# Kernel tuning notes

Hardware: AMD Instinct MI355X
Metric: run time of the kernel (lower is better)

Reference implementation:

```python
import jax, jax.numpy as jnp
import numpy as np

NEG_INF = -1e9  # matches torch masked_fill(-1000000000.0)


def setup_inputs() -> dict:
    key = jax.random.key(0)
    kv, kk, kq, km, kw, kb = jax.random.split(key, 6)
    B, Lq, Lk, D = 8, 1024, 4096, 1024  # Lq must equal D (transpose-then-merge quirk)
    v = jax.random.normal(kv, (B, Lk, D), dtype=jnp.float32)
    k = jax.random.normal(kk, (B, Lk, D), dtype=jnp.float32)
    q = jax.random.normal(kq, (B, Lq, D), dtype=jnp.float32)
    mask = jax.random.randint(km, (B, Lq, Lk), 0, 2) > 0  # bool, True = masked out
    W_merge = jax.random.normal(kw, (D, D), dtype=jnp.float32) / np.sqrt(D)
    b_merge = jax.random.normal(kb, (D,), dtype=jnp.float32) * 0.02
    return {"v": v, "k": k, "q": q, "mask": mask, "W_merge": W_merge, "b_merge": b_merge}


def reference(v, k, q, mask, W_merge, b_merge):
    d_k = q.shape[-1]
    scale = 1.0 / jnp.sqrt(jnp.asarray(d_k, dtype=q.dtype))
    # scores: [B, Lq, Lk]
    scores = jnp.einsum('bqd,bkd->bqk', q, k) * scale
    scores = jnp.where(mask, jnp.asarray(NEG_INF, dtype=scores.dtype), scores)
    att_map = jax.nn.softmax(scores, axis=-1)  # dropout = identity in eval
    atted = jnp.einsum('bqk,bkd->bqd', att_map, v)  # [B, Lq, D]
    atted = jnp.swapaxes(atted, -1, -2)  # [B, D, Lq]; Lq == hid_dim
    # nn.Linear: y = x @ W^T + b
    return jnp.einsum('bdl,ol->bdo', atted, W_merge) + b_merge
```

## Files before the change

kernel.cpp:

```cpp
#include <hip/hip_runtime.h>
#include <stdint.h>

typedef __attribute__((ext_vector_type(4))) float f32x4;
typedef __attribute__((ext_vector_type(8))) short bf16x8;
typedef __attribute__((ext_vector_type(4))) short bf16x4v;
typedef __attribute__((ext_vector_type(4))) unsigned int u32x4;

#define NBATCH 8
#define LQS    1024
#define LKS    4096
#define DDIM   1024
#define QKSCALE 0.03125f
#define NEGINF -1000000000.0f
#define BK 64

__device__ __forceinline__ short f2bf(float x) {
    unsigned u = __builtin_bit_cast(unsigned, x);
    unsigned r = (u + 0x7fffu + ((u >> 16) & 1u)) >> 16;
    return (short)r;
}
__device__ __forceinline__ float bf2f(short s) {
    unsigned u = ((unsigned)(unsigned short)s) << 16;
    return __builtin_bit_cast(float, u);
}

__device__ __forceinline__ bf16x8 cvt8(const float* f) {
    const u32x4* u = (const u32x4*)f;
    const u32x4 a = u[0], b = u[1];
    union { unsigned w[4]; bf16x8 v; } c;
    c.w[0] = __builtin_amdgcn_perm(a[1], a[0], 0x07060302u);
    c.w[1] = __builtin_amdgcn_perm(a[3], a[2], 0x07060302u);
    c.w[2] = __builtin_amdgcn_perm(b[1], b[0], 0x07060302u);
    c.w[3] = __builtin_amdgcn_perm(b[3], b[2], 0x07060302u);
    return c.v;
}

__device__ __forceinline__ void g2l16(const void* g, void* lds) {
    __builtin_amdgcn_global_load_lds(
        (const __attribute__((address_space(1))) unsigned int*)g,
        (__attribute__((address_space(3))) unsigned int*)lds,
        16, 0, 0);
}

__device__ __forceinline__ int xcd_swz(int bid, int nwg) {
    return (bid & 7) * (nwg >> 3) + (bid >> 3);
}

__global__ void detect_kernel(const unsigned char* __restrict__ mb,
                              int* __restrict__ flags) {
    if (threadIdx.x != 0 || blockIdx.x != 0) return;
    int is_i32 = 1;
    for (int i = 0; i < 256; ++i) {
        if ((i & 3) != 0 && mb[i] != 0) { is_i32 = 0; break; }
    }
    flags[0] = is_i32;
}

__global__ __launch_bounds__(256) void cvt_kernel(
    const float* __restrict__ src, short* __restrict__ dst, int n8) {
    const int stride = gridDim.x * 256;
    for (int i = blockIdx.x * 256 + threadIdx.x; i < n8; i += stride)
        ((bf16x8*)dst)[i] = cvt8(src + (size_t)i * 8);
}

__global__ __launch_bounds__(256) void transv_kernel(
    const float* __restrict__ V, short* __restrict__ VT) {
    __shared__ short LDSt[64 * 72];
    const int tid = threadIdx.x;
    const int cb  = blockIdx.x >> 10;
    const int t   = blockIdx.x & 1023;
    const int kt  = t >> 4, dt = t & 15;
    const int k0  = kt * 64, d0 = dt * 64;
    const float* Vb  = V  + (size_t)cb * LKS * DDIM;
    short*       VTb = VT + (size_t)cb * ((size_t)DDIM * LKS);

    const int r  = tid >> 4;
    const int cp = (tid & 15) * 4;
#pragma unroll
    for (int rr = 0; rr < 4; ++rr) {
        const int row = rr * 16 + r;
        const f32x4 v = *(const f32x4*)(Vb + (size_t)(k0 + row) * DDIM + d0 + cp);
#pragma unroll
        for (int i = 0; i < 4; ++i) LDSt[(cp + i) * 72 + row] = f2bf(v[i]);
    }
    __syncthreads();
    const int dr = tid >> 2;
    const int kq = (tid & 3) * 16;
    const bf16x8 o0 = *(const bf16x8*)&LDSt[dr * 72 + kq];
    const bf16x8 o1 = *(const bf16x8*)&LDSt[dr * 72 + kq + 8];
    short* dst = VTb + (size_t)(d0 + dr) * LKS + k0 + kq;
    *(bf16x8*)dst       = o0;
    *(bf16x8*)(dst + 8) = o1;
}

__device__ __forceinline__ void stage_half(const short* gbase, int ld,
                                           short* ldshalf, int tid) {
    const int r0 = tid >> 3;
    const int gc = (tid & 7) ^ (r0 & 7);
    const short* s0 = gbase + (size_t)r0 * ld + gc * 8;
    const short* s1 = gbase + (size_t)(r0 + 64) * ld + gc * 8;
    g2l16(s0, ldshalf + (tid & 0x1C0) * 8);
    g2l16(s1, ldshalf + 4096 + (tid & 0x1C0) * 8);
}

__device__ __forceinline__ bf16x8 rdfrag(const short* lds, int base, int r, int c) {
    return *(const bf16x8*)&lds[base + r * 64 + ((c ^ (r & 7)) << 3)];
}

#define MFMA16(d, a, b) d = __builtin_amdgcn_mfma_f32_16x16x32_bf16(a, b, d, 0, 0, 0)

#define PHASE(MF0, STAGE, TAIL)                                             \
    {                                                                       \
        bf16x8 a00 = rdfrag(lds, aBase, (MF0) * 16 + lo, g);                \
        bf16x8 a01 = rdfrag(lds, aBase, (MF0) * 16 + lo, 4 + g);            \
        bf16x8 a10 = rdfrag(lds, aBase, (MF0) * 16 + 16 + lo, g);          \
        bf16x8 a11 = rdfrag(lds, aBase, (MF0) * 16 + 16 + lo, 4 + g);      \
        STAGE;                                                              \
        asm volatile("s_barrier" ::: "memory");                             \
        __builtin_amdgcn_s_setprio(1);                                      \
        _Pragma("unroll")                                                   \
        for (int nf = 0; nf < 4; ++nf) {                                    \
            MFMA16(acc[(MF0)][nf], a00, bfr[nf][0]);                        \
            MFMA16(acc[(MF0)][nf], a01, bfr[nf][1]);                        \
            MFMA16(acc[(MF0) + 1][nf], a10, bfr[nf][0]);                    \
            MFMA16(acc[(MF0) + 1][nf], a11, bfr[nf][1]);                    \
        }                                                                   \
        __builtin_amdgcn_s_setprio(0);                                      \
        TAIL;                                                               \
        asm volatile("s_barrier" ::: "memory");                             \
    }


template <int EPI>
__device__ __forceinline__ void gemm8p_body(
    const short* __restrict__ A, int lda,
    const short* __restrict__ B, int ldb,
    void* __restrict__ C, int ldc,
    const float* __restrict__ bias,
    int m0, int n0, int NK, float scale, short* lds) {

    const int tid = threadIdx.x;
    const int w = tid >> 6, lane = tid & 63;
    const int lo = lane & 15, g = lane >> 4;
    const int wr = w >> 2, wc = w & 3;

    const short* gA0 = A + (size_t)m0 * lda;
    const short* gA1 = A + (size_t)(m0 + 128) * lda;
    const short* gB0 = B + (size_t)n0 * ldb;
    const short* gB1 = B + (size_t)(n0 + 128) * ldb;

    f32x4 acc[8][4];
#pragma unroll
    for (int mf = 0; mf < 8; ++mf)
#pragma unroll
        for (int nf = 0; nf < 4; ++nf) acc[mf][nf] = (f32x4){0.f, 0.f, 0.f, 0.f};

    stage_half(gA0, lda, lds + 0,     tid);
    stage_half(gA1, lda, lds + 8192,  tid);
    stage_half(gB0, ldb, lds + 16384, tid);
    stage_half(gB1, ldb, lds + 24576, tid);
    stage_half(gB0 + BK, ldb, lds + 32768 + 16384, tid);
    stage_half(gB1 + BK, ldb, lds + 32768 + 24576, tid);
    asm volatile("s_waitcnt vmcnt(4)" ::: "memory");
    asm volatile("s_barrier" ::: "memory");

    for (int kt = 0; kt < NK; ++kt) {
        const int cb = (kt & 1) << 15;
        const int ob = cb ^ 32768;
        const int aBase = cb + wr * 8192;
        const int bBase = cb + 16384 + (wc >> 1) * 8192;
        const int brow  = (wc & 1) * 64;
        const int kA = (kt + 1) * BK, kB = (kt + 2) * BK;
        const bool doA = (kt + 1) < NK, doB = (kt + 2) < NK;

        bf16x8 bfr[4][2];
#pragma unroll
        for (int nf = 0; nf < 4; ++nf) {
            bfr[nf][0] = rdfrag(lds, bBase, brow + nf * 16 + lo, g);
            bfr[nf][1] = rdfrag(lds, bBase, brow + nf * 16 + lo, 4 + g);
        }
        PHASE(0, if (doA) stage_half(gA0 + kA, lda, lds + ob, tid), )
        PHASE(2, if (doA) stage_half(gA1 + kA, lda, lds + ob + 8192, tid), )
        PHASE(4, if (doB) stage_half(gB0 + kB, ldb, lds + cb + 16384, tid), )
        PHASE(6, if (doB) stage_half(gB1 + kB, ldb, lds + cb + 24576, tid),
                 {
                     if (doB) { asm volatile("s_waitcnt vmcnt(4)" ::: "memory"); }
                     else     { asm volatile("s_waitcnt vmcnt(0)" ::: "memory"); }
                 })
    }

    if constexpr (EPI == 0 || EPI == 2) {
#pragma unroll
        for (int nf = 0; nf < 4; ++nf) {
            const int col = n0 + wc * 64 + nf * 16 + lo;
            float bv = 0.f;
            if constexpr (EPI == 2) bv = bias[col];
#pragma unroll
            for (int mf = 0; mf < 8; ++mf) {
#pragma unroll
                for (int rr = 0; rr < 4; ++rr) {
                    const size_t oa =
                        (size_t)(m0 + wr * 128 + mf * 16 + g * 4 + rr) * ldc + col;
                    if constexpr (EPI == 0) ((float*)C)[oa] = acc[mf][nf][rr] * scale;
                    else                    ((float*)C)[oa] = acc[mf][nf][rr] + bv;
                }
            }
        }
    } else {
        const float sc_ = (EPI == 3) ? scale : 1.f;
#pragma unroll
        for (int half = 0; half < 2; ++half) {
            if (wr == half) {
#pragma unroll
                for (int nf = 0; nf < 4; ++nf)
#pragma unroll
                    for (int mf = 0; mf < 8; ++mf)
#pragma unroll
                        for (int rr = 0; rr < 4; ++rr)
                            lds[(mf * 16 + g * 4 + rr) * 264 + wc * 64 + nf * 16 + lo] =
                                f2bf(acc[mf][nf][rr] * sc_);
            }
            __syncthreads();
#pragma unroll
            for (int it = 0; it < 8; ++it) {
                const int idx = it * 512 + tid;
                const int r_  = idx >> 5;
                const int c_  = (idx & 31) * 8;
                *(bf16x8*)((short*)C + (size_t)(m0 + half * 128 + r_) * ldc + n0 + c_) =
                    *(const bf16x8*)&lds[r_ * 264 + c_];
            }
            __syncthreads();
        }
    }
}

template <int EPI>
__device__ __forceinline__ void gemm8p_n128(
    const short* __restrict__ A, int lda,
    const short* __restrict__ B, int ldb,
    void* __restrict__ C, int ldc,
    const float* __restrict__ bias,
    int m0, int n0, int NK, float scale, short* lds) {

    const int tid = threadIdx.x;
    const int w = tid >> 6, lane = tid & 63;
    const int lo = lane & 15, g = lane >> 4;
    const int wr = w >> 1, wc = w & 1;

    const short* gA0 = A + (size_t)m0 * lda;
    const short* gA1 = A + (size_t)(m0 + 128) * lda;
    const short* gB0 = B + (size_t)n0 * ldb;

    f32x4 acc[4][4];
#pragma unroll
    for (int mf = 0; mf < 4; ++mf)
#pragma unroll
        for (int nf = 0; nf < 4; ++nf) acc[mf][nf] = (f32x4){0.f, 0.f, 0.f, 0.f};

    stage_half(gA0, lda, lds + 0,    tid);
    stage_half(gA1, lda, lds + 8192, tid);
    stage_half(gB0, ldb, lds + 16384, tid);
    stage_half(gB0 + BK, ldb, lds + 24576 + 16384, tid);
    asm volatile("s_waitcnt vmcnt(2)" ::: "memory");
    asm volatile("s_barrier" ::: "memory");

    for (int kt = 0; kt < NK; ++kt) {
        const int cbuf = (kt & 1) * 24576;
        const int obuf = cbuf ^ 24576;
        const int aBase = cbuf + (wr >> 1) * 8192 + (wr & 1) * 4096;
        const int bBase = cbuf + 16384 + wc * 4096;
        const int kA = (kt + 1) * BK, kB = (kt + 2) * BK;
        const bool doA = (kt + 1) < NK, doB = (kt + 2) < NK;

        bf16x8 bfr[4][2];
#pragma unroll
        for (int nf = 0; nf < 4; ++nf) {
            bfr[nf][0] = rdfrag(lds, bBase, nf * 16 + lo, g);
            bfr[nf][1] = rdfrag(lds, bBase, nf * 16 + lo, 4 + g);
        }
        PHASE(0, {
            if (doA) {
                stage_half(gA0 + kA, lda, lds + obuf, tid);
                stage_half(gA1 + kA, lda, lds + obuf + 8192, tid);
            }
        }, )
        PHASE(2, {
            if (doB) stage_half(gB0 + kB, ldb, lds + cbuf + 16384, tid);
        }, {
            if (doB) { asm volatile("s_waitcnt vmcnt(2)" ::: "memory"); }
            else     { asm volatile("s_waitcnt vmcnt(0)" ::: "memory"); }
        })
    }

    if constexpr (EPI == 0 || EPI == 2) {
#pragma unroll
        for (int nf = 0; nf < 4; ++nf) {
            const int col = n0 + wc * 64 + nf * 16 + lo;
            float bv = 0.f;
            if constexpr (EPI == 2) bv = bias[col];
#pragma unroll
            for (int mf = 0; mf < 4; ++mf) {
#pragma unroll
                for (int rr = 0; rr < 4; ++rr) {
                    const size_t oa =
                        (size_t)(m0 + wr * 64 + mf * 16 + g * 4 + rr) * ldc + col;
                    if constexpr (EPI == 0) ((float*)C)[oa] = acc[mf][nf][rr] * scale;
                    else                    ((float*)C)[oa] = acc[mf][nf][rr] + bv;
                }
            }
        }
    } else {
        const float sc_ = (EPI == 3) ? scale : 1.f;
#pragma unroll
        for (int nf = 0; nf < 4; ++nf)
#pragma unroll
            for (int mf = 0; mf < 4; ++mf)
#pragma unroll
                for (int rr = 0; rr < 4; ++rr)
                    lds[(wr * 64 + mf * 16 + g * 4 + rr) * 136 + wc * 64 + nf * 16 + lo] =
                        f2bf(acc[mf][nf][rr] * sc_);
        __syncthreads();
#pragma unroll
        for (int it = 0; it < 8; ++it) {
            const int idx = it * 512 + tid;
            const int r_  = idx >> 4;
            const int c_  = (idx & 15) * 8;
            *(bf16x8*)((short*)C + (size_t)(m0 + r_) * ldc + n0 + c_) =
                *(const bf16x8*)&lds[r_ * 136 + c_];
        }
    }
}

__global__ __launch_bounds__(512, 2) void gemm1_kernel(
    const short* __restrict__ Qb, const short* __restrict__ Kb,
    short* __restrict__ Sb) {
    __shared__ __align__(16) short lds[65536];
    const int bid = xcd_swz(blockIdx.x, gridDim.x);
    const int cb = bid >> 6;
    const int t  = bid & 63;
    gemm8p_body<3>(Qb + (size_t)cb * LQS * DDIM, DDIM,
                   Kb + (size_t)cb * LKS * DDIM, DDIM,
                   Sb + (size_t)cb * ((size_t)LQS * LKS), LKS, nullptr,
                   (t >> 4) * 256, (t & 15) * 256, DDIM / BK, QKSCALE, lds);
}

__global__ __launch_bounds__(512, 2) void gemm2_kernel(
    const short* __restrict__ VT, const short* __restrict__ Pd,
    short* __restrict__ attedT) {
    __shared__ __align__(16) short lds[49152];
    const int bid = xcd_swz(blockIdx.x, gridDim.x);
    const int cb = bid >> 5;
    const int t  = bid & 31;
    gemm8p_n128<1>(VT + (size_t)cb * ((size_t)DDIM * LKS), LKS,
                   Pd + (size_t)cb * ((size_t)LQS * LKS), LKS,
                   attedT + (size_t)cb * ((size_t)DDIM * LQS), LQS, nullptr,
                   (t >> 3) * 256, (t & 7) * 128, LKS / BK, 1.f, lds);
}

__global__ __launch_bounds__(512, 2) void merge_kernel(
    const short* __restrict__ attedT, const short* __restrict__ Wb,
    const float* __restrict__ bias, float* __restrict__ out) {
    __shared__ __align__(16) short lds[49152];
    const int bid = xcd_swz(blockIdx.x, gridDim.x);
    const int mt = bid >> 3;
    const int nt = bid & 7;
    gemm8p_n128<2>(attedT, DDIM, Wb, DDIM, out, DDIM, bias,
                   mt * 256, nt * 128, DDIM / BK, 1.f, lds);
}

__global__ __launch_bounds__(256) void softmax_kernel(
    const short* __restrict__ Sb, short* __restrict__ Pd,
    const void* __restrict__ mask, const int* __restrict__ flags, int c0) {
    __shared__ float red[4];
    const int tid = threadIdx.x, w = tid >> 6, lane = tid & 63;
    const int cb = blockIdx.x >> 10;
    const int q  = blockIdx.x & 1023;
    const int mflag = flags[0];

    const short* Srow = Sb + ((size_t)cb * LQS + q) * LKS;
    const size_t roff = ((size_t)(c0 + cb) * LQS + q) * LKS;
    const size_t m4   = roff >> 2;

    float sc[16];
#pragma unroll
    for (int j = 0; j < 2; ++j) {
        const int i8 = j * 256 + tid;
        const bf16x8 sv = ((const bf16x8*)Srow)[i8];
        int mm[8];
        if (mflag) {
            const int4 a = ((const int4*)mask)[m4 + 2 * i8];
            const int4 b = ((const int4*)mask)[m4 + 2 * i8 + 1];
            mm[0] = a.x; mm[1] = a.y; mm[2] = a.z; mm[3] = a.w;
            mm[4] = b.x; mm[5] = b.y; mm[6] = b.z; mm[7] = b.w;
        } else {
            const uchar4 a = ((const uchar4*)mask)[m4 + 2 * i8];
            const uchar4 b = ((const uchar4*)mask)[m4 + 2 * i8 + 1];
            mm[0] = a.x; mm[1] = a.y; mm[2] = a.z; mm[3] = a.w;
            mm[4] = b.x; mm[5] = b.y; mm[6] = b.z; mm[7] = b.w;
        }
#pragma unroll
        for (int i = 0; i < 8; ++i)
            sc[j * 8 + i] = mm[i] ? NEGINF : bf2f(sv[i]);
    }

    float lm = -INFINITY;
#pragma unroll
    for (int i = 0; i < 16; ++i) lm = fmaxf(lm, sc[i]);
#pragma unroll
    for (int off = 1; off < 64; off <<= 1) lm = fmaxf(lm, __shfl_xor(lm, off));
    if (lane == 0) red[w] = lm;
    __syncthreads();
    const float m = fmaxf(fmaxf(red[0], red[1]), fmaxf(red[2], red[3]));

    float p[16], ls = 0.f;
#pragma unroll
    for (int i = 0; i < 16; ++i) { p[i] = __expf(sc[i] - m); ls += p[i]; }
#pragma unroll
    for (int off = 1; off < 64; off <<= 1) ls += __shfl_xor(ls, off);
    __syncthreads();
    if (lane == 0) red[w] = ls;
    __syncthreads();
    const float inv = 1.f / (red[0] + red[1] + red[2] + red[3]);

    short* Prow = Pd + ((size_t)cb * LQS + q) * LKS;
#pragma unroll
    for (int j = 0; j < 2; ++j) {
        bf16x8 pv;
#pragma unroll
        for (int i = 0; i < 8; ++i) pv[i] = f2bf(p[j * 8 + i] * inv);
        ((bf16x8*)Prow)[j * 256 + tid] = pv;
    }
}

extern "C" void kernel_launch(void* const* d_in, const int* in_sizes, int n_in,
                              void* d_out, int out_size, void* d_ws, size_t ws_size,
                              hipStream_t stream) {
    const float* v    = (const float*)d_in[0];
    const float* k    = (const float*)d_in[1];
    const float* q    = (const float*)d_in[2];
    const void*  mask = d_in[3];
    const float* Wm   = (const float*)d_in[4];
    const float* bias = (const float*)d_in[5];
    float* out = (float*)d_out;

    const size_t base = 4096 + (2ull << 20);
    int nb = 0;
    for (int cand = 8; cand >= 1; cand >>= 1)
        if (base + (size_t)cand * (36ull << 20) <= ws_size) { nb = cand; break; }
    if (!nb) return;

    int*   flags = (int*)d_ws;
    short* Wb    = (short*)((char*)d_ws + 4096);
    char*  ar    = (char*)d_ws + base;
    short* Sb     = (short*)ar;
    short* VTbuf  = (short*)(ar + ((size_t)nb << 24));
    short* attedT = (short*)(ar + ((size_t)nb << 24) + ((size_t)nb << 23));
    short* Qb     = (short*)(ar + ((size_t)nb << 24) + ((size_t)nb << 23) + ((size_t)nb << 21));
    short* Kb     = (short*)(ar + ((size_t)nb << 24) + ((size_t)nb << 23) + 2 * ((size_t)nb << 21));
    short* Pd     = Kb;

    hipLaunchKernelGGL(detect_kernel, dim3(1), dim3(64), 0, stream,
                       (const unsigned char*)mask, flags);
    hipLaunchKernelGGL(cvt_kernel, dim3(512), dim3(256), 0, stream,
                       Wm, Wb, (int)(DDIM * DDIM / 8));

    for (int c0 = 0; c0 < NBATCH; c0 += nb) {
        const float* vc = v + (size_t)c0 * LKS * DDIM;
        const float* kc = k + (size_t)c0 * LKS * DDIM;
        const float* qc = q + (size_t)c0 * LQS * DDIM;
        float*       oc = out + (size_t)c0 * DDIM * LQS;

        hipLaunchKernelGGL(cvt_kernel, dim3(1024), dim3(256), 0, stream,
                           qc, Qb, nb * (LQS * DDIM / 8));
        hipLaunchKernelGGL(cvt_kernel, dim3(2048), dim3(256), 0, stream,
                           kc, Kb, nb * (LKS * DDIM / 8));
        hipLaunchKernelGGL(transv_kernel, dim3(nb * 1024), dim3(256), 0, stream,
                           vc, VTbuf);
        hipLaunchKernelGGL(gemm1_kernel, dim3(nb * 64), dim3(512), 0, stream,
                           Qb, Kb, Sb);
        hipLaunchKernelGGL(softmax_kernel, dim3(nb * 1024), dim3(256), 0, stream,
                           Sb, Pd, mask, flags, c0);
        hipLaunchKernelGGL(gemm2_kernel, dim3(nb * 32), dim3(512), 0, stream,
                           VTbuf, Pd, attedT);
        hipLaunchKernelGGL(merge_kernel, dim3(nb * 32), dim3(512), 0, stream,
                           attedT, Wb, bias, oc);
    }
}
```

Before: 322.4 us.

## Use 4-wave blocks with larger per-wave tiles for gemm2 and merge

Replaces the 8-wave 256x128 GEMM used by gemm2 and the merge projection with a 4-wave variant. Each wave now computes 128x64 (eight M-fragments), and the A/B staging is split across four phases. This raises the MFMA work per LDS fragment read and per barrier, and the MFMA order is changed so consecutive instructions do not depend on each other. In exchange it uses many more accumulator registers and allows only one block per CU, with half the threads issuing loads. Combined with a small grid (nb*32 blocks), that could hurt latency hiding.

```diff
diff --git a/kernel.cpp b/kernel.cpp
--- a/kernel.cpp
+++ b/kernel.cpp
@@ -101,6 +101,17 @@
     const short* s1 = gbase + (size_t)(r0 + 64) * ld + gc * 8;
     g2l16(s0, ldshalf + (tid & 0x1C0) * 8);
     g2l16(s1, ldshalf + 4096 + (tid & 0x1C0) * 8);
+}
+
+__device__ __forceinline__ void stage_half_256(const short* gbase, int ld,
+                                               short* ldshalf, int tid) {
+#pragma unroll
+    for (int p = 0; p < 4; ++p) {
+        const int r0 = p * 32 + (tid >> 3);
+        const int gc = (tid & 7) ^ (r0 & 7);
+        g2l16(gbase + (size_t)r0 * ld + gc * 8,
+              ldshalf + p * 2048 + (tid & 0xC0) * 8);
+    }
 }
 
 __device__ __forceinline__ bf16x8 rdfrag(const short* lds, int base, int r, int c) {
@@ -121,8 +132,11 @@
         _Pragma("unroll")                                                   \
         for (int nf = 0; nf < 4; ++nf) {                                    \
             MFMA16(acc[(MF0)][nf], a00, bfr[nf][0]);                        \
+            MFMA16(acc[(MF0) + 1][nf], a10, bfr[nf][0]);                    \
+        }                                                                   \
+        _Pragma("unroll")                                                   \
+        for (int nf = 0; nf < 4; ++nf) {                                    \
             MFMA16(acc[(MF0)][nf], a01, bfr[nf][1]);                        \
-            MFMA16(acc[(MF0) + 1][nf], a10, bfr[nf][0]);                    \
             MFMA16(acc[(MF0) + 1][nf], a11, bfr[nf][1]);                    \
         }                                                                   \
         __builtin_amdgcn_s_setprio(0);                                      \
@@ -235,7 +249,7 @@
 }
 
 template <int EPI>
-__device__ __forceinline__ void gemm8p_n128(
+__device__ __forceinline__ void gemm4w_body(
     const short* __restrict__ A, int lda,
     const short* __restrict__ B, int ldb,
     void* __restrict__ C, int ldc,
@@ -251,45 +265,42 @@
     const short* gA1 = A + (size_t)(m0 + 128) * lda;
     const short* gB0 = B + (size_t)n0 * ldb;
 
-    f32x4 acc[4][4];
-#pragma unroll
-    for (int mf = 0; mf < 4; ++mf)
+    f32x4 acc[8][4];
+#pragma unroll
+    for (int mf = 0; mf < 8; ++mf)
 #pragma unroll
         for (int nf = 0; nf < 4; ++nf) acc[mf][nf] = (f32x4){0.f, 0.f, 0.f, 0.f};
 
-    stage_half(gA0, lda, lds + 0,    tid);
-    stage_half(gA1, lda, lds + 8192, tid);
-    stage_half(gB0, ldb, lds + 16384, tid);
-    stage_half(gB0 + BK, ldb, lds + 24576 + 16384, tid);
-    asm volatile("s_waitcnt vmcnt(2)" ::: "memory");
+    stage_half_256(gA0, lda, lds + 0,     tid);
+    stage_half_256(gA1, lda, lds + 8192,  tid);
+    stage_half_256(gB0, ldb, lds + 16384, tid);
+    stage_half_256(gB0 + BK, ldb, lds + 24576 + 16384, tid);
+    asm volatile("s_waitcnt vmcnt(4)" ::: "memory");
     asm volatile("s_barrier" ::: "memory");
 
     for (int kt = 0; kt < NK; ++kt) {
         const int cbuf = (kt & 1) * 24576;
         const int obuf = cbuf ^ 24576;
-        const int aBase = cbuf + (wr >> 1) * 8192 + (wr & 1) * 4096;
-        const int bBase = cbuf + 16384 + wc * 4096;
+        const int aBase = cbuf + wr * 8192;
+        const int bBase = cbuf + 16384;
+        const int brow  = wc * 64;
         const int kA = (kt + 1) * BK, kB = (kt + 2) * BK;
         const bool doA = (kt + 1) < NK, doB = (kt + 2) < NK;
 
         bf16x8 bfr[4][2];
 #pragma unroll
         for (int nf = 0; nf < 4; ++nf) {
-            bfr[nf][0] = rdfrag(lds, bBase, nf * 16 + lo, g);
-            bfr[nf][1] = rdfrag(lds, bBase, nf * 16 + lo, 4 + g);
-        }
-        PHASE(0, {
-            if (doA) {
-                stage_half(gA0 + kA, lda, lds + obuf, tid);
-                stage_half(gA1 + kA, lda, lds + obuf + 8192, tid);
-            }
-        }, )
-        PHASE(2, {
-            if (doB) stage_half(gB0 + kB, ldb, lds + cbuf + 16384, tid);
-        }, {
-            if (doB) { asm volatile("s_waitcnt vmcnt(2)" ::: "memory"); }
-            else     { asm volatile("s_waitcnt vmcnt(0)" ::: "memory"); }
-        })
+            bfr[nf][0] = rdfrag(lds, bBase, brow + nf * 16 + lo, g);
+            bfr[nf][1] = rdfrag(lds, bBase, brow + nf * 16 + lo, 4 + g);
+        }
+        PHASE(0, if (doA) stage_half_256(gA0 + kA, lda, lds + obuf, tid), )
+        PHASE(2, if (doA) stage_half_256(gA1 + kA, lda, lds + obuf + 8192, tid), )
+        PHASE(4, if (doB) stage_half_256(gB0 + kB, ldb, lds + cbuf + 16384, tid), )
+        PHASE(6, ,
+                 {
+                     if (doB) { asm volatile("s_waitcnt vmcnt(4)" ::: "memory"); }
+                     else     { asm volatile("s_waitcnt vmcnt(0)" ::: "memory"); }
+                 })
     }
 
     if constexpr (EPI == 0 || EPI == 2) {
@@ -299,11 +310,11 @@
             float bv = 0.f;
             if constexpr (EPI == 2) bv = bias[col];
 #pragma unroll
-            for (int mf = 0; mf < 4; ++mf) {
+            for (int mf = 0; mf < 8; ++mf) {
 #pragma unroll
                 for (int rr = 0; rr < 4; ++rr) {
                     const size_t oa =
-                        (size_t)(m0 + wr * 64 + mf * 16 + g * 4 + rr) * ldc + col;
+                        (size_t)(m0 + wr * 128 + mf * 16 + g * 4 + rr) * ldc + col;
                     if constexpr (EPI == 0) ((float*)C)[oa] = acc[mf][nf][rr] * scale;
                     else                    ((float*)C)[oa] = acc[mf][nf][rr] + bv;
                 }
@@ -312,21 +323,27 @@
     } else {
         const float sc_ = (EPI == 3) ? scale : 1.f;
 #pragma unroll
-        for (int nf = 0; nf < 4; ++nf)
-#pragma unroll
-            for (int mf = 0; mf < 4; ++mf)
-#pragma unroll
-                for (int rr = 0; rr < 4; ++rr)
-                    lds[(wr * 64 + mf * 16 + g * 4 + rr) * 136 + wc * 64 + nf * 16 + lo] =
-                        f2bf(acc[mf][nf][rr] * sc_);
-        __syncthreads();
-#pragma unroll
-        for (int it = 0; it < 8; ++it) {
-            const int idx = it * 512 + tid;
-            const int r_  = idx >> 4;
-            const int c_  = (idx & 15) * 8;
-            *(bf16x8*)((short*)C + (size_t)(m0 + r_) * ldc + n0 + c_) =
-                *(const bf16x8*)&lds[r_ * 136 + c_];
+        for (int half = 0; half < 2; ++half) {
+            if (wr == half) {
+#pragma unroll
+                for (int nf = 0; nf < 4; ++nf)
+#pragma unroll
+                    for (int mf = 0; mf < 8; ++mf)
+#pragma unroll
+                        for (int rr = 0; rr < 4; ++rr)
+                            lds[(mf * 16 + g * 4 + rr) * 136 + wc * 64 + nf * 16 + lo] =
+                                f2bf(acc[mf][nf][rr] * sc_);
+            }
+            __syncthreads();
+#pragma unroll
+            for (int it = 0; it < 8; ++it) {
+                const int idx = it * 256 + tid;
+                const int r_  = idx >> 4;
+                const int c_  = (idx & 15) * 8;
+                *(bf16x8*)((short*)C + (size_t)(m0 + half * 128 + r_) * ldc + n0 + c_) =
+                    *(const bf16x8*)&lds[r_ * 136 + c_];
+            }
+            __syncthreads();
         }
     }
 }
@@ -344,27 +361,27 @@
                    (t >> 4) * 256, (t & 15) * 256, DDIM / BK, QKSCALE, lds);
 }
 
-__global__ __launch_bounds__(512, 2) void gemm2_kernel(
+__global__ __launch_bounds__(256, 1) void gemm2_kernel(
     const short* __restrict__ VT, const short* __restrict__ Pd,
     short* __restrict__ attedT) {
     __shared__ __align__(16) short lds[49152];
     const int bid = xcd_swz(blockIdx.x, gridDim.x);
     const int cb = bid >> 5;
     const int t  = bid & 31;
-    gemm8p_n128<1>(VT + (size_t)cb * ((size_t)DDIM * LKS), LKS,
+    gemm4w_body<1>(VT + (size_t)cb * ((size_t)DDIM * LKS), LKS,
                    Pd + (size_t)cb * ((size_t)LQS * LKS), LKS,
                    attedT + (size_t)cb * ((size_t)DDIM * LQS), LQS, nullptr,
                    (t >> 3) * 256, (t & 7) * 128, LKS / BK, 1.f, lds);
 }
 
-__global__ __launch_bounds__(512, 2) void merge_kernel(
+__global__ __launch_bounds__(256, 1) void merge_kernel(
     const short* __restrict__ attedT, const short* __restrict__ Wb,
     const float* __restrict__ bias, float* __restrict__ out) {
     __shared__ __align__(16) short lds[49152];
     const int bid = xcd_swz(blockIdx.x, gridDim.x);
     const int mt = bid >> 3;
     const int nt = bid & 7;
-    gemm8p_n128<2>(attedT, DDIM, Wb, DDIM, out, DDIM, bias,
+    gemm4w_body<2>(attedT, DDIM, Wb, DDIM, out, DDIM, bias,
                    mt * 256, nt * 128, DDIM / BK, 1.f, lds);
 }
 
@@ -480,9 +497,9 @@
                            Qb, Kb, Sb);
         hipLaunchKernelGGL(softmax_kernel, dim3(nb * 1024), dim3(256), 0, stream,
                            Sb, Pd, mask, flags, c0);
-        hipLaunchKernelGGL(gemm2_kernel, dim3(nb * 32), dim3(512), 0, stream,
+        hipLaunchKernelGGL(gemm2_kernel, dim3(nb * 32), dim3(256), 0, stream,
                            VTbuf, Pd, attedT);
-        hipLaunchKernelGGL(merge_kernel, dim3(nb * 32), dim3(512), 0, stream,
+        hipLaunchKernelGGL(merge_kernel, dim3(nb * 32), dim3(256), 0, stream,
                            attedT, Wb, bias, oc);
     }
 }
```

Result: slower. 339.9 us (+5.4%).
